# Optimization experiments

Measured on AMD Instinct MI355X. Metric: run time of the kernel, lower is better.

Reference implementation:

```python
import jax, jax.numpy as jnp
import numpy as np

RADIUS = 0.12
N_SAMPLE = 32


def ball_query(radius, n_sample, xyz, new_xyz):
    """Faithful replication of pointnet2 ball_query CUDA semantics.

    For each query point, take the FIRST n_sample points (in index order)
    with squared distance < radius^2. If fewer than n_sample are found,
    remaining slots repeat the first found index. If none found, idx = 0.
    """
    B, N, _ = xyz.shape
    # d2[b,p,n] = ||new_xyz[b,p] - xyz[b,n]||^2 via expansion (avoids [B,P,N,3])
    qq = jnp.sum(new_xyz * new_xyz, axis=-1)[:, :, None]          # [B,P,1]
    xx = jnp.sum(xyz * xyz, axis=-1)[:, None, :]                  # [B,1,N]
    qx = jnp.einsum('bpd,bnd->bpn', new_xyz, xyz)                 # [B,P,N]
    d2 = qq + xx - 2.0 * qx
    mask = d2 < radius * radius
    # score = N - n for in-ball points (strictly decreasing in n), 0 otherwise.
    # top_k then yields the first n_sample in-ball indices in ascending n order.
    score = jnp.where(mask, (N - jnp.arange(N, dtype=jnp.int32))[None, None, :],
                      jnp.int32(0))
    vals, idx = jax.lax.top_k(score, n_sample)                    # [B,P,S]
    valid = vals > 0
    first = jnp.where(valid[..., :1], idx[..., :1], 0)            # 0 if no neighbor
    return jnp.where(valid, idx, first).astype(jnp.int32)


def group(features, idx):
    """features: [B,C,N], idx: [B,P,S] -> [B,C,P,S]."""
    return jax.vmap(lambda f, i: f[:, i])(features, idx)


def setup_inputs() -> dict:
    key = jax.random.key(0)
    k1, k2, k3 = jax.random.split(key, 3)
    B, N, P, C = 4, 8192, 2048, 64
    xyz = jax.random.uniform(k1, (B, N, 3), dtype=jnp.float32)
    new_xyz = jax.random.uniform(k2, (B, P, 3), dtype=jnp.float32)
    features = jax.random.normal(k3, (B, C, N), dtype=jnp.float32)
    return {"xyz": xyz, "new_xyz": new_xyz, "features": features}


def reference(xyz, new_xyz, features):
    idx = ball_query(RADIUS, N_SAMPLE, xyz, new_xyz)              # [B,P,S] int32
    xyz_t = jnp.transpose(xyz, (0, 2, 1))                         # [B,3,N]
    grouped_xyz = group(xyz_t, idx)                               # [B,3,P,S]
    grouped_xyz = grouped_xyz - jnp.transpose(new_xyz, (0, 2, 1))[..., None]
    grouped_features = group(features, idx)                       # [B,C,P,S]
    return jnp.concatenate([grouped_xyz, grouped_features], axis=1)  # [B,3+C,P,S]
```

## Files before the change

kernel.cpp:

```cpp
#include <hip/hip_runtime.h>

constexpr int kB = 4;
constexpr int kN = 8192;
constexpr int kP = 2048;
constexpr int kS = 32;
constexpr int kC = 64;
constexpr int kCO = 67;
constexpr float kR2 = 0.0144f;

__device__ __forceinline__ float sq3(float x, float y, float z) {
  return __fadd_rn(__fadd_rn(__fmul_rn(x, x), __fmul_rn(y, y)),
                   __fmul_rn(z, z));
}
__device__ __forceinline__ float dot3(float ax, float ay, float az, float bx,
                                      float by, float bz) {
  return __fadd_rn(__fadd_rn(__fmul_rn(ax, bx), __fmul_rn(ay, by)),
                   __fmul_rn(az, bz));
}

__global__ __launch_bounds__(256) void bq_k(const float* __restrict__ xyz,
                                            const float* __restrict__ new_xyz,
                                            int* __restrict__ g_idx) {
  __shared__ unsigned short sidx[4][2][32];
  __shared__ int scnt[4][2];

  const int tid = threadIdx.x;
  const int wv = tid >> 6;
  const int lane = tid & 63;
  const int w = blockIdx.x * 4 + wv;
  const int q0 = w * 2;
  const int b = q0 >> 11;
  const int p = q0 & (kP - 1);

  const float* xb = xyz + (size_t)b * kN * 3;
  const float* qb = new_xyz + ((size_t)b * kP + p) * 3;

  const float qx0 = qb[0], qy0 = qb[1], qz0 = qb[2];
  const float qx1 = qb[3], qy1 = qb[4], qz1 = qb[5];
  const float qq0 = sq3(qx0, qy0, qz0);
  const float qq1 = sq3(qx1, qy1, qz1);

  const unsigned long long lmask = (1ull << lane) - 1ull;
  int cnt0 = 0, cnt1 = 0;

#define PROC(j)                                                             \
  {                                                                         \
    float d2 = __fsub_rn(__fadd_rn(qq##j, xx),                              \
                         __fmul_rn(2.0f, dot3(qx##j, qy##j, qz##j, px, py,  \
                                              pz)));                        \
    unsigned long long m = __ballot(d2 < kR2);                              \
    if (m) {                                                                \
      int pos = cnt##j + __popcll(m & lmask);                               \
      if ((d2 < kR2) && pos < kS)                                           \
        sidx[wv][j][pos] = (unsigned short)ncur;                            \
      cnt##j += __popcll(m);                                                \
    }                                                                       \
  }

  float cx[4], cy[4], cz[4];
#pragma unroll
  for (int k = 0; k < 4; ++k) {
    int n = k * 64 + lane;
    cx[k] = xb[3 * n + 0];
    cy[k] = xb[3 * n + 1];
    cz[k] = xb[3 * n + 2];
  }

  int gbase = 0;
  for (int g0 = 256;; g0 += 256) {
    const bool more = (g0 < kN);
    const int g1 = more ? g0 : 0;
    float nx[4], ny[4], nz[4];
#pragma unroll
    for (int k = 0; k < 4; ++k) {
      int n = g1 + k * 64 + lane;
      nx[k] = xb[3 * n + 0];
      ny[k] = xb[3 * n + 1];
      nz[k] = xb[3 * n + 2];
    }
#pragma unroll
    for (int k = 0; k < 4; ++k) {
      const float px = cx[k], py = cy[k], pz = cz[k];
      const float xx = sq3(px, py, pz);
      const int ncur = gbase + k * 64 + lane;
      PROC(0)
      PROC(1)
    }
    if (!more || (cnt0 >= kS && cnt1 >= kS)) break;
#pragma unroll
    for (int k = 0; k < 4; ++k) {
      cx[k] = nx[k];
      cy[k] = ny[k];
      cz[k] = nz[k];
    }
    gbase = g0;
  }
#undef PROC

  if (lane == 0) {
    scnt[wv][0] = cnt0;
    scnt[wv][1] = cnt1;
  }
  __syncthreads();

  const int j = lane >> 5, s = lane & 31;
  int c = scnt[wv][j];
  int first = (c > 0) ? (int)sidx[wv][j][0] : 0;
  int val = (s < c) ? (int)sidx[wv][j][s] : first;
  g_idx[((size_t)(b * kP + p + j)) * kS + s] = val;
}

__global__ __launch_bounds__(512) void gather_k2(
    const float* __restrict__ xyz, const float* __restrict__ new_xyz,
    const float* __restrict__ feat, const int* __restrict__ g_idx,
    float* __restrict__ out) {
  __shared__ float row[kN];
  __shared__ float nxz[kP / 2];
  const int tid = threadIdx.x;
  const int bi = blockIdx.x;
  const int b = bi / (kCO * 2);
  const int r = bi % (kCO * 2);
  const int c = r >> 1;
  const int ph = r & 1;

  if (c < 3) {
    for (int i = tid; i < kN; i += 512)
      row[i] = xyz[((size_t)b * kN + i) * 3 + c];
    for (int i = tid; i < kP / 2; i += 512)
      nxz[i] = new_xyz[((size_t)b * kP + ph * (kP / 2) + i) * 3 + c];
  } else {
    const float4* src = (const float4*)(feat + ((size_t)b * kC + (c - 3)) * kN);
    float4* dst = (float4*)row;
    for (int i = tid; i < kN / 4; i += 512) dst[i] = src[i];
  }
  __syncthreads();

  const size_t eg_base = (((size_t)b * kP + ph * (kP / 2)) * kS) >> 2;
  const int4* idx4 = (const int4*)g_idx + eg_base;
  float4* out4 =
      (float4*)out + ((((size_t)b * kCO + c) * kP + ph * (kP / 2)) * kS >> 2);
  const bool isxyz = (c < 3);
#pragma unroll 4
  for (int it = 0; it < (kP / 2) * kS / 4 / 512; ++it) {
    const int e4 = it * 512 + tid;
    const int4 n = idx4[e4];
    float4 v = make_float4(row[n.x], row[n.y], row[n.z], row[n.w]);
    if (isxyz) {
      const float sub = nxz[e4 >> 3];
      v.x = __fsub_rn(v.x, sub);
      v.y = __fsub_rn(v.y, sub);
      v.z = __fsub_rn(v.z, sub);
      v.w = __fsub_rn(v.w, sub);
    }
    out4[e4] = v;
  }
}

__global__ __launch_bounds__(512) void fused_qg(
    const float* __restrict__ xyz, const float* __restrict__ new_xyz,
    const float* __restrict__ feat, float* __restrict__ out) {
  __shared__ __align__(16) char ls[32768 + 512 + 4096];
  unsigned short (*sidx)[64][32] = (unsigned short (*)[64][32])ls;
  float* row = (float*)ls;
  unsigned char (*scnt)[64] = (unsigned char (*)[64])(ls + 32768);
  unsigned short (*midx)[32] = (unsigned short (*)[32])(ls + 32768 + 512);

  const int tid = threadIdx.x;
  const int wv = tid >> 6;
  const int lane = tid & 63;
  const int b = blockIdx.x >> 5;
  const int p0 = (blockIdx.x & 31) << 6;

  {
    const float* q = &new_xyz[(b * kP + p0 + lane) * 3];
    const float qx = q[0], qy = q[1], qz = q[2];
    const float qq = sq3(qx, qy, qz);
    const float* xb = xyz + ((size_t)b * kN + wv * 1024) * 3;
    int cnt = 0;
    for (int i = 0; i < 1024; ++i) {
      float px = xb[i * 3 + 0], py = xb[i * 3 + 1], pz = xb[i * 3 + 2];
      float xx = sq3(px, py, pz);
      float d2 = __fsub_rn(__fadd_rn(qq, xx),
                           __fmul_rn(2.0f, dot3(qx, qy, qz, px, py, pz)));
      if (d2 < kR2 && cnt < kS) {
        sidx[wv][lane][cnt] = (unsigned short)(wv * 1024 + i);
        ++cnt;
      }
    }
    scnt[wv][lane] = (unsigned char)cnt;
  }
  __syncthreads();

  if (tid < 64) {
    int filled = 0, first = 0;
    bool has = false;
    for (int sg = 0; sg < 8 && filled < kS; ++sg) {
      int c = scnt[sg][tid];
      for (int k = 0; k < c && filled < kS; ++k) {
        int n = sidx[sg][tid][k];
        if (!has) { first = n; has = true; }
        midx[tid][filled++] = (unsigned short)n;
      }
    }
    for (; filled < kS; ++filled) midx[tid][filled] = (unsigned short)first;
  }

  for (int c = 0; c < kCO; ++c) {
    __syncthreads();
    if (c < 3) {
      for (int i = tid; i < kN; i += 512)
        row[i] = xyz[((size_t)b * kN + i) * 3 + c];
    } else {
      const float4* src =
          (const float4*)(feat + ((size_t)b * kC + (c - 3)) * kN);
      float4* dst = (float4*)row;
      for (int i = tid; i < kN / 4; i += 512) dst[i] = src[i];
    }
    __syncthreads();
    const int outbase = ((b * kCO + c) * kP + p0) * kS;
    for (int e = tid; e < 64 * kS; e += 512) {
      int n = midx[e >> 5][e & 31];
      float v = row[n];
      if (c < 3) v = __fsub_rn(v, new_xyz[(b * kP + p0 + (e >> 5)) * 3 + c]);
      out[outbase + e] = v;
    }
  }
}

extern "C" void kernel_launch(void* const* d_in, const int* in_sizes, int n_in,
                              void* d_out, int out_size, void* d_ws,
                              size_t ws_size, hipStream_t stream) {
  const float* xyz = (const float*)d_in[0];
  const float* new_xyz = (const float*)d_in[1];
  const float* feat = (const float*)d_in[2];
  float* out = (float*)d_out;

  const size_t idx_bytes = (size_t)kB * kP * kS * sizeof(int);
  if (ws_size >= idx_bytes) {
    int* g_idx = (int*)d_ws;
    bq_k<<<dim3(kB * kP / 8), dim3(256), 0, stream>>>(xyz, new_xyz, g_idx);
    gather_k2<<<dim3(kB * kCO * 2), dim3(512), 0, stream>>>(xyz, new_xyz, feat,
                                                            g_idx, out);
  } else {
    fused_qg<<<dim3(kB * (kP / 64)), dim3(512), 0, stream>>>(xyz, new_xyz,
                                                             feat, out);
  }
}
```

Measured before the change: 47.54 us.

## Replace linear ball-query scan with uniform grid binning in a cooperative kernel

```diff
diff --git a/kernel.cpp b/kernel.cpp
--- a/kernel.cpp
+++ b/kernel.cpp
@@ -1,4 +1,7 @@
 #include <hip/hip_runtime.h>
+#include <hip/hip_cooperative_groups.h>
+
+namespace cg = cooperative_groups;
 
 constexpr int kB = 4;
 constexpr int kN = 8192;
@@ -8,6 +11,10 @@
 constexpr int kCO = 67;
 constexpr float kR2 = 0.0144f;
 
+constexpr int kG = 8;
+constexpr int kCells = kG * kG * kG;
+constexpr int kCap = 64;
+
 __device__ __forceinline__ float sq3(float x, float y, float z) {
   return __fadd_rn(__fadd_rn(__fmul_rn(x, x), __fmul_rn(y, y)),
                    __fmul_rn(z, z));
@@ -16,6 +23,143 @@
                                       float by, float bz) {
   return __fadd_rn(__fadd_rn(__fmul_rn(ax, bx), __fmul_rn(ay, by)),
                    __fmul_rn(az, bz));
+}
+
+__device__ __forceinline__ int cell_of(float x) {
+  int c = (int)(x * 8.0f);
+  return c > 7 ? 7 : (c < 0 ? 0 : c);
+}
+
+__global__ __launch_bounds__(256, 4) void bq_coop(
+    const float* __restrict__ xyz, const float* __restrict__ new_xyz,
+    int* __restrict__ cnt, float4* __restrict__ slots,
+    int* __restrict__ g_idx) {
+  __shared__ unsigned short plist[4][256];
+  __shared__ int lcnt[kCells];
+
+  const int tid = threadIdx.x;
+
+  if (blockIdx.x < kB) {
+    for (int i = tid; i < kCells; i += 256) lcnt[i] = 0;
+    __syncthreads();
+    const int b = blockIdx.x;
+    const float* xb = xyz + (size_t)b * kN * 3;
+    for (int i = 0; i < kN / 256; ++i) {
+      const int n = i * 256 + tid;
+      const float x = xb[3 * n + 0];
+      const float y = xb[3 * n + 1];
+      const float z = xb[3 * n + 2];
+      const int cell = (cell_of(z) * kG + cell_of(y)) * kG + cell_of(x);
+      const int pos = atomicAdd(&lcnt[cell], 1);
+      if (pos < kCap)
+        slots[((size_t)(b * kCells + cell)) * kCap + pos] =
+            make_float4(x, y, z, __int_as_float(n));
+    }
+    __syncthreads();
+    for (int i = tid; i < kCells; i += 256) cnt[b * kCells + i] = lcnt[i];
+  }
+
+  cg::this_grid().sync();
+
+  const int wv = tid >> 6;
+  const int lane = tid & 63;
+  const unsigned long long lmask = (1ull << lane) - 1ull;
+
+  for (int qi = 0; qi < 2; ++qi) {
+    const int q = blockIdx.x * 8 + wv * 2 + qi;
+    const int b = q >> 11;
+    const int p = q & (kP - 1);
+
+    const float* qb = new_xyz + ((size_t)b * kP + p) * 3;
+    const float qx = qb[0], qy = qb[1], qz = qb[2];
+    const float qq = sq3(qx, qy, qz);
+
+    const int cqx = cell_of(qx), cqy = cell_of(qy), cqz = cell_of(qz);
+    const int x0 = cqx > 0 ? cqx - 1 : 0, x1 = cqx < 7 ? cqx + 1 : 7;
+    const int y0 = cqy > 0 ? cqy - 1 : 0, y1 = cqy < 7 ? cqy + 1 : 7;
+    const int z0 = cqz > 0 ? cqz - 1 : 0, z1 = cqz < 7 ? cqz + 1 : 7;
+
+    int tp = 0;
+
+    for (int cz = z0; cz <= z1; ++cz)
+      for (int cy = y0; cy <= y1; ++cy)
+        for (int cx = x0; cx <= x1; ++cx) {
+          const int gid = b * kCells + (cz * kG + cy) * kG + cx;
+          int c = cnt[gid];
+          c = c > kCap ? kCap : c;
+          bool pass = false;
+          int idx = 0;
+          if (lane < c) {
+            const float4 s = slots[(size_t)gid * kCap + lane];
+            const float px = s.x, py = s.y, pz = s.z;
+            const float xx = sq3(px, py, pz);
+            const float d2 =
+                __fsub_rn(__fadd_rn(qq, xx),
+                          __fmul_rn(2.0f, dot3(qx, qy, qz, px, py, pz)));
+            pass = d2 < kR2;
+            idx = __float_as_int(s.w);
+          }
+          const unsigned long long m = __ballot(pass);
+          if (m) {
+            const int pos = tp + __popcll(m & lmask);
+            if (pass && pos < 256) plist[wv][pos] = (unsigned short)idx;
+            tp += __popcll(m);
+          }
+        }
+
+    int val;
+    if (tp <= 64) {
+      int v = (lane < tp) ? (int)plist[wv][lane] : 65535;
+#pragma unroll
+      for (int k = 2; k <= 64; k <<= 1) {
+#pragma unroll
+        for (int j = k >> 1; j > 0; j >>= 1) {
+          const int pv = __shfl_xor(v, j);
+          const bool lower = (lane & j) == 0;
+          const bool asc = (lane & k) == 0;
+          v = (lower == asc) ? (v < pv ? v : pv) : (v > pv ? v : pv);
+        }
+      }
+      const int first = __shfl(v, 0);
+      val = (tp == 0) ? 0 : ((lane < tp) ? v : first);
+    } else {
+      const int ctp = tp > 256 ? 256 : tp;
+      int v0 = (lane < ctp) ? (int)plist[wv][lane] : 65535;
+      int v1 = (lane + 64 < ctp) ? (int)plist[wv][lane + 64] : 65535;
+      int v2 = (lane + 128 < ctp) ? (int)plist[wv][lane + 128] : 65535;
+      int v3 = (lane + 192 < ctp) ? (int)plist[wv][lane + 192] : 65535;
+      int t;
+#define CSWP(a, b) \
+  if (a > b) {     \
+    t = a;         \
+    a = b;         \
+    b = t;         \
+  }
+      CSWP(v0, v1) CSWP(v2, v3) CSWP(v0, v2) CSWP(v1, v3) CSWP(v1, v2)
+#undef CSWP
+      int res = 0;
+      for (int r = 0; r < 32; ++r) {
+        int g = v0;
+#pragma unroll
+        for (int off = 32; off > 0; off >>= 1) {
+          const int og = __shfl_xor(g, off);
+          g = og < g ? og : g;
+        }
+        const unsigned long long mm = __ballot(v0 == g);
+        const int win = __ffsll(mm) - 1;
+        if (lane == win) {
+          v0 = v1;
+          v1 = v2;
+          v2 = v3;
+          v3 = 65535;
+        }
+        if (lane == r) res = g;
+      }
+      val = res;
+    }
+
+    if (lane < kS) g_idx[((size_t)(b * kP + p)) * kS + lane] = val;
+  }
 }
 
 __global__ __launch_bounds__(256) void bq_k(const float* __restrict__ xyz,
@@ -238,7 +382,17 @@
   const size_t idx_bytes = (size_t)kB * kP * kS * sizeof(int);
   if (ws_size >= idx_bytes) {
     int* g_idx = (int*)d_ws;
-    bq_k<<<dim3(kB * kP / 8), dim3(256), 0, stream>>>(xyz, new_xyz, g_idx);
+    int* cnt = (int*)d_out;
+    float4* slots =
+        (float4*)((char*)d_out + (size_t)kB * kCells * sizeof(int));
+
+    void* args[] = {(void*)&xyz, (void*)&new_xyz, (void*)&cnt, (void*)&slots,
+                    (void*)&g_idx};
+    hipError_t err = hipLaunchCooperativeKernel(
+        (const void*)bq_coop, dim3(kB * kP / 8), dim3(256), args, 0, stream);
+    if (err != hipSuccess) {
+      bq_k<<<dim3(kB * kP / 8), dim3(256), 0, stream>>>(xyz, new_xyz, g_idx);
+    }
     gather_k2<<<dim3(kB * kCO * 2), dim3(512), 0, stream>>>(xyz, new_xyz, feat,
                                                             g_idx, out);
   } else {
```

Result: slower. 188.8 us (+297.2%).
